# Optimization experiments

Measured on AMD Instinct MI355X. Metric: run time of the kernel, lower is better.

Reference implementation:

```python
import jax, jax.numpy as jnp
import numpy as np

COMMITMENT_COST = 0.25
NUM_EMBEDDINGS = 4096
EMBEDDING_DIM = 256


def setup_inputs() -> dict:
    key = jax.random.key(0)
    kx, ke = jax.random.split(key)
    x = jax.random.normal(kx, (64, 1024, EMBEDDING_DIM), dtype=jnp.float32)
    # nn.Embedding weight initialized uniform(-1/K, 1/K)
    emb = jax.random.uniform(ke, (NUM_EMBEDDINGS, EMBEDDING_DIM), dtype=jnp.float32,
                             minval=-1.0 / NUM_EMBEDDINGS, maxval=1.0 / NUM_EMBEDDINGS)
    return {"x": x, "emb": emb}


def reference(x, emb):
    D = emb.shape[1]
    flat_x = x.reshape(-1, D)                                    # [N, D]
    distances = (jnp.sum(flat_x * flat_x, axis=1, keepdims=True)
                 - 2.0 * flat_x @ emb.T
                 + jnp.sum(emb * emb, axis=1))
    indices = jnp.argmin(distances, axis=1)                      # [N]
    quantized = emb[indices].reshape(x.shape)                    # [..., D]
    e_latent_loss = jnp.mean((jax.lax.stop_gradient(quantized) - x) ** 2)
    q_latent_loss = jnp.mean((quantized - jax.lax.stop_gradient(x)) ** 2)
    loss = q_latent_loss + COMMITMENT_COST * e_latent_loss
    # straight-through estimator
    quantized = x + jax.lax.stop_gradient(quantized - x)
    return quantized, loss, indices[:, None]
```

## Files before the change

### kernel.cpp

```cpp
#include <hip/hip_runtime.h>
#include <math.h>

#define DIMD 256
#define KCODES 4096
#define NROWS 65536
#define QN (NROWS * DIMD)

constexpr int P1_BM = 64;
constexpr int P1_BN = 128;
constexpr int NT    = KCODES / P1_BN;
constexpr float TAU2 = 7.5e-4f;
constexpr float TAU2B = TAU2 + 1e-5f;
constexpr int CAP   = 48;
constexpr int NS    = 8;

typedef __attribute__((ext_vector_type(8))) short bf16x8;
typedef __attribute__((ext_vector_type(4))) float f32x4;

__device__ __forceinline__ unsigned short f2bf(float f) {
    unsigned int u = __builtin_bit_cast(unsigned int, f);
    u += 0x7fffu + ((u >> 16) & 1u);
    return (unsigned short)(u >> 16);
}

__device__ __forceinline__ float opaque(float v) {
    asm volatile("" : "+v"(v));
    return v;
}

__device__ __forceinline__ void gload_lds16(const void* g, void* l) {
    __builtin_amdgcn_global_load_lds(
        (const __attribute__((address_space(1))) unsigned int*)g,
        (__attribute__((address_space(3))) unsigned int*)l, 16, 0, 0);
}

__device__ __forceinline__ float np_sumsq_256(const float* __restrict__ p) {
    float total = 0.0f;
    #pragma unroll
    for (int half = 0; half < 2; ++half) {
        const float* b = p + half * 128;
        float r[8];
        #pragma unroll
        for (int j = 0; j < 8; ++j) {
            const float v = b[j];
            r[j] = opaque(v * v);
        }
        for (int i = 8; i < 128; i += 8) {
            #pragma unroll
            for (int j = 0; j < 8; ++j) {
                const float v = b[i + j];
                r[j] += opaque(v * v);
            }
        }
        const float res = ((r[0] + r[1]) + (r[2] + r[3])) + ((r[4] + r[5]) + (r[6] + r[7]));
        total = (half == 0) ? res : (total + res);
    }
    return total;
}

__global__ void sx_kernel(const float* __restrict__ x, float* __restrict__ sx) {
    const int row = blockIdx.x * blockDim.x + threadIdx.x;
    sx[row] = np_sumsq_256(x + (size_t)row * DIMD);
}

__global__ void se_kernel(const float* __restrict__ emb, float* __restrict__ se) {
    const int k = blockIdx.x * blockDim.x + threadIdx.x;
    se[k] = np_sumsq_256(emb + (size_t)k * DIMD);
}

__global__ void conv_emb_kernel(const float* __restrict__ emb, unsigned short* __restrict__ embh) {
    const int i = blockIdx.x * blockDim.x + threadIdx.x;
    const float4 v = ((const float4*)emb)[i];
    ushort4 h;
    h.x = f2bf(v.x); h.y = f2bf(v.y); h.z = f2bf(v.z); h.w = f2bf(v.w);
    ((ushort4*)embh)[i] = h;
}

__global__ __launch_bounds__(256, 2)
void pass1_kernel(const float* __restrict__ x, const unsigned short* __restrict__ embh,
                  unsigned int* __restrict__ cand, int* __restrict__ cnt_out) {
    __shared__ unsigned short Bs[2][8192];
    __shared__ float part[4][32];
    __shared__ float tilemax[P1_BM];
    __shared__ int   cnts[P1_BM];

    const int t    = threadIdx.x;
    const int w    = t >> 6;
    const int lane = t & 63;
    const int quad = lane >> 4;
    const int lm   = lane & 15;
    const int wr   = w >> 1;
    const int wc   = w & 1;
    const int row0 = blockIdx.x * P1_BM;

    if (t < P1_BM) cnts[t] = 0;

    bf16x8 afr[2][8];
    #pragma unroll
    for (int f = 0; f < 2; ++f) {
        const float* xr = x + (size_t)(row0 + wr * 32 + f * 16 + lm) * DIMD + quad * 8;
        #pragma unroll
        for (int c = 0; c < 8; ++c) {
            const float4 v0 = *(const float4*)(xr + c * 32);
            const float4 v1 = *(const float4*)(xr + c * 32 + 4);
            bf16x8 h;
            h[0] = (short)f2bf(v0.x); h[1] = (short)f2bf(v0.y);
            h[2] = (short)f2bf(v0.z); h[3] = (short)f2bf(v0.w);
            h[4] = (short)f2bf(v1.x); h[5] = (short)f2bf(v1.y);
            h[6] = (short)f2bf(v1.z); h[7] = (short)f2bf(v1.w);
            afr[f][c] = h;
        }
    }

    auto stage = [&](int buf, int m) {
        const int c0  = (m >> 2) * P1_BN;
        const int kcb = (m & 3) * 64;
        #pragma unroll
        for (int i = 0; i < 4; ++i) {
            const int seg  = i * 4 + w;
            const int code = seg * 8 + (lane >> 3);
            const int kk   = ((lane & 7) ^ ((lane >> 3) & 7)) * 8;
            const unsigned short* src = embh + (size_t)(c0 + code) * DIMD + kcb + kk;
            gload_lds16(src, &Bs[buf][seg * 512]);
        }
    };

    stage(0, 0);
    asm volatile("s_waitcnt vmcnt(0)" ::: "memory");
    __syncthreads();

    float rmg[2][4];
    #pragma unroll
    for (int f = 0; f < 2; ++f)
        #pragma unroll
        for (int reg = 0; reg < 4; ++reg) rmg[f][reg] = -INFINITY;

    int buf = 0;
    for (int tile = 0; tile < NT; ++tile) {
        const int c0 = tile * P1_BN;
        f32x4 acc[2][4];
        #pragma unroll
        for (int f = 0; f < 2; ++f)
            #pragma unroll
            for (int g = 0; g < 4; ++g) acc[f][g] = (f32x4){0.f, 0.f, 0.f, 0.f};

        #pragma unroll
        for (int kb = 0; kb < 4; ++kb) {
            const int m = tile * 4 + kb;
            if (m < NT * 4 - 1) stage(buf ^ 1, m + 1);

            #pragma unroll
            for (int ks = 0; ks < 2; ++ks) {
                bf16x8 b[4];
                #pragma unroll
                for (int g = 0; g < 4; ++g) {
                    const int j = wc * 64 + g * 16 + lm;
                    b[g] = *(const bf16x8*)
                        &Bs[buf][j * 64 + ((((ks << 2) + quad) ^ (lm & 7)) << 3)];
                }
                #pragma unroll
                for (int f = 0; f < 2; ++f)
                    #pragma unroll
                    for (int g = 0; g < 4; ++g)
                        acc[f][g] = __builtin_amdgcn_mfma_f32_16x16x32_bf16(
                            afr[f][kb * 2 + ks], b[g], acc[f][g], 0, 0, 0);
            }

            if (kb == 3) {
                #pragma unroll
                for (int f = 0; f < 2; ++f) {
                    f32x4 mm4;
                    #pragma unroll
                    for (int reg = 0; reg < 4; ++reg) {
                        float mm = fmaxf(fmaxf(acc[f][0][reg], acc[f][1][reg]),
                                         fmaxf(acc[f][2][reg], acc[f][3][reg]));
                        #pragma unroll
                        for (int off = 1; off < 16; off <<= 1)
                            mm = fmaxf(mm, __shfl_xor(mm, off, 64));
                        mm4[reg] = mm;
                    }
                    if (lm == 0)
                        *(f32x4*)&part[w][f * 16 + quad * 4] = mm4;
                }
            }

            asm volatile("s_waitcnt vmcnt(0)" ::: "memory");
            __syncthreads();
            buf ^= 1;
        }

        if (t < P1_BM) {
            const int trh = t >> 5, loc = t & 31;
            tilemax[t] = fmaxf(part[trh * 2][loc], part[trh * 2 + 1][loc]);
        }
        __syncthreads();

        #pragma unroll
        for (int f = 0; f < 2; ++f) {
            const f32x4 tm = *(const f32x4*)&tilemax[wr * 32 + f * 16 + quad * 4];
            #pragma unroll
            for (int reg = 0; reg < 4; ++reg) {
                rmg[f][reg] = fmaxf(rmg[f][reg], tm[reg]);
                const float thr = rmg[f][reg] - TAU2;
                const int r = wr * 32 + f * 16 + quad * 4 + reg;
                #pragma unroll
                for (int g = 0; g < 4; ++g) {
                    const float dv = acc[f][g][reg];
                    if (dv > thr) {
                        const int slot = atomicAdd(&cnts[r], 1);
                        if (slot < CAP) {
                            const unsigned int ub =
                                __builtin_bit_cast(unsigned int, fmaxf(dv, 0.0f));
                            cand[(size_t)(row0 + r) * CAP + slot] =
                                (ub & 0xFFFFF000u) |
                                (unsigned int)(c0 + wc * 64 + g * 16 + lm);
                        }
                    }
                }
            }
        }
    }
    __syncthreads();
    if (t < P1_BM) cnt_out[row0 + t] = (cnts[t] > CAP) ? -1 : cnts[t];
}

__global__ __launch_bounds__(256, 2)
void pass2_kernel(const float* __restrict__ x, const float* __restrict__ emb,
                  const float* __restrict__ sx, const float* __restrict__ se,
                  const unsigned int* __restrict__ cand, const int* __restrict__ cnt,
                  float* __restrict__ out, float* __restrict__ partial) {
    __shared__ float4 xsh[4][64];
    __shared__ float4 esh[4][NS][65];
    const int w = threadIdx.x >> 6, lane = threadIdx.x & 63;
    const int row = blockIdx.x * 4 + w;
    const int n = cnt[row];
    const float sxr = sx[row];
    const float4* emb4 = (const float4*)emb;

    const float4 myx = ((const float4*)(x + (size_t)row * DIMD))[lane];
    xsh[w][lane] = myx;
    const float4* xs4 = &xsh[w][0];

    float bestd = INFINITY;
    int   bestc = 0x7fffffff;

    if (n >= 1 && n <= CAP) {
        float dtil = -INFINITY;
        int   code = 0;
        if (lane < n) {
            const unsigned int word = cand[(size_t)row * CAP + lane];
            dtil = __builtin_bit_cast(float, word & 0xFFFFF000u);
            code = (int)(word & 0xFFFu);
        }
        float mx = dtil;
        #pragma unroll
        for (int off = 1; off < 64; off <<= 1)
            mx = fmaxf(mx, __shfl_xor(mx, off, 64));
        const bool active = (lane < n) && (dtil > mx - TAU2B);
        const unsigned long long mask = __ballot(active);
        const int nact = __popcll(mask);
        const int slot = __popcll(mask & ((1ull << lane) - 1ull));
        unsigned long long mm = mask;
        const int ns = nact < NS ? nact : NS;
        for (int i = 0; i < ns; ++i) {
            const int li = __ffsll((unsigned long long)mm) - 1;
            mm &= mm - 1;
            const int bc = __shfl(code, li, 64);
            esh[w][i][lane] = emb4[(size_t)bc * 64 + lane];
        }
        if (active) {
            float a = 0.0f;
            if (slot < NS) {
                const float4* ep4 = &esh[w][slot][0];
                #pragma unroll
                for (int d4 = 0; d4 < DIMD / 4; ++d4) {
                    const float4 ev = ep4[d4];
                    const float4 xv = xs4[d4];
                    a = fmaf(xv.x, ev.x, a);
                    a = fmaf(xv.y, ev.y, a);
                    a = fmaf(xv.z, ev.z, a);
                    a = fmaf(xv.w, ev.w, a);
                }
            } else {
                const float4* ep4 = (const float4*)(emb + (size_t)code * DIMD);
                #pragma unroll
                for (int d4 = 0; d4 < DIMD / 4; ++d4) {
                    const float4 ev = ep4[d4];
                    const float4 xv = xs4[d4];
                    a = fmaf(xv.x, ev.x, a);
                    a = fmaf(xv.y, ev.y, a);
                    a = fmaf(xv.z, ev.z, a);
                    a = fmaf(xv.w, ev.w, a);
                }
            }
            const float t1 = sxr - 2.0f * a;
            bestd = t1 + se[code];
            bestc = code;
        }
    } else {
        for (int c = lane; c < KCODES; c += 64) {
            const float* ep = emb + (size_t)c * DIMD;
            float a = 0.0f;
            for (int d4 = 0; d4 < DIMD / 4; ++d4) {
                const float4 xv = xs4[d4];
                const float4 ev = ((const float4*)ep)[d4];
                a = fmaf(xv.x, ev.x, a);
                a = fmaf(xv.y, ev.y, a);
                a = fmaf(xv.z, ev.z, a);
                a = fmaf(xv.w, ev.w, a);
            }
            const float t1 = sxr - 2.0f * a;
            const float dd = t1 + se[c];
            if (dd < bestd || (dd == bestd && c < bestc)) { bestd = dd; bestc = c; }
        }
    }
    #pragma unroll
    for (int off = 32; off > 0; off >>= 1) {
        const float od = __shfl_down(bestd, off, 64);
        const int   oc = __shfl_down(bestc, off, 64);
        if (od < bestd || (od == bestd && oc < bestc)) { bestd = od; bestc = oc; }
    }
    bestc = __shfl(bestc, 0, 64);

    const float4 e4 = emb4[(size_t)bestc * 64 + lane];
    ((float4*)(out + (size_t)row * DIMD))[lane] = e4;
    const float dx = e4.x - myx.x, dy = e4.y - myx.y,
                dz = e4.z - myx.z, dw = e4.w - myx.w;
    float s = dx * dx + dy * dy + dz * dz + dw * dw;
    #pragma unroll
    for (int off = 32; off > 0; off >>= 1) s += __shfl_down(s, off, 64);
    if (lane == 0) {
        partial[row] = s;
        out[QN + 1 + row] = (float)bestc;
    }
}

__global__ void loss_reduce_kernel(const float* __restrict__ partial, float* __restrict__ out) {
    const int t = threadIdx.x;
    double s = 0.0;
    for (int i = t; i < NROWS; i += 256) s += (double)partial[i];
    __shared__ double tsum[256];
    tsum[t] = s;
    __syncthreads();
    #pragma unroll
    for (int off = 128; off > 0; off >>= 1) {
        if (t < off) tsum[t] += tsum[t + off];
        __syncthreads();
    }
    if (t == 0) out[QN] = (float)(tsum[0] * (1.25 / (double)QN));
}

extern "C" void kernel_launch(void* const* d_in, const int* in_sizes, int n_in,
                              void* d_out, int out_size, void* d_ws, size_t ws_size,
                              hipStream_t stream) {
    const float* x   = (const float*)d_in[0];
    const float* emb = (const float*)d_in[1];
    float* out = (float*)d_out;

    char* ws = (char*)d_ws;
    unsigned short* embh = (unsigned short*)ws;           ws += (size_t)KCODES * DIMD * 2;
    float* sx  = (float*)ws;                              ws += (size_t)NROWS * 4;
    float* se  = (float*)ws;                              ws += (size_t)KCODES * 4;
    unsigned int* cand = (unsigned int*)ws;               ws += (size_t)NROWS * CAP * 4;
    int*   cnt  = (int*)ws;                               ws += (size_t)NROWS * 4;
    float* partial = (float*)ws;

    conv_emb_kernel<<<KCODES * DIMD / 4 / 256, 256, 0, stream>>>(emb, embh);
    sx_kernel<<<NROWS / 256, 256, 0, stream>>>(x, sx);
    se_kernel<<<KCODES / 256, 256, 0, stream>>>(emb, se);
    pass1_kernel<<<NROWS / P1_BM, 256, 0, stream>>>(x, embh, cand, cnt);
    pass2_kernel<<<NROWS / 4, 256, 0, stream>>>(x, emb, sx, se, cand, cnt, out, partial);
    loss_reduce_kernel<<<1, 256, 0, stream>>>(partial, out);
}
```

Measured before the change: 793.3 us.

## Triple-buffer pass1 LDS staging, cooperative row norms, LDS-staged pass2 candidates

Pass1 moves from a double to a triple LDS buffer that prefetches two k-blocks ahead, using partial vmcnt waits so global loads overlap the MFMA work. The sx/se norm kernels now use 8 lanes per row with shuffle reductions in place of one thread per row, which gives coalesced loads. Pass2 loads candidate embeddings into LDS with global_load_lds, drops the padding column, reuses the staged winning row for the output, and raises occupancy to 4 blocks. The norm reduction order changes, which may shift sums slightly versus the numpy-matching order, and the partial vmcnt counts have to match the number of loads issued per stage.

```diff
diff --git a/kernel.cpp b/kernel.cpp
--- a/kernel.cpp
+++ b/kernel.cpp
@@ -17,6 +17,10 @@
 typedef __attribute__((ext_vector_type(8))) short bf16x8;
 typedef __attribute__((ext_vector_type(4))) float f32x4;
 
+#define VM8() asm volatile("s_waitcnt vmcnt(8)" ::: "memory")
+#define VM4() asm volatile("s_waitcnt vmcnt(4)" ::: "memory")
+#define VM0() asm volatile("s_waitcnt vmcnt(0)" ::: "memory")
+
 __device__ __forceinline__ unsigned short f2bf(float f) {
     unsigned int u = __builtin_bit_cast(unsigned int, f);
     u += 0x7fffu + ((u >> 16) & 1u);
@@ -34,38 +38,50 @@
         (__attribute__((address_space(3))) unsigned int*)l, 16, 0, 0);
 }
 
-__device__ __forceinline__ float np_sumsq_256(const float* __restrict__ p) {
+__global__ void sx_kernel(const float* __restrict__ x, float* __restrict__ sx) {
+    const int j   = threadIdx.x & 7;
+    const int row = blockIdx.x * 32 + (threadIdx.x >> 3);
+    const float* p = x + (size_t)row * DIMD;
     float total = 0.0f;
     #pragma unroll
     for (int half = 0; half < 2; ++half) {
         const float* b = p + half * 128;
-        float r[8];
-        #pragma unroll
-        for (int j = 0; j < 8; ++j) {
-            const float v = b[j];
-            r[j] = opaque(v * v);
-        }
+        const float v0 = b[j];
+        float r = opaque(v0 * v0);
+        #pragma unroll
         for (int i = 8; i < 128; i += 8) {
-            #pragma unroll
-            for (int j = 0; j < 8; ++j) {
-                const float v = b[i + j];
-                r[j] += opaque(v * v);
-            }
-        }
-        const float res = ((r[0] + r[1]) + (r[2] + r[3])) + ((r[4] + r[5]) + (r[6] + r[7]));
+            const float v = b[i + j];
+            r += opaque(v * v);
+        }
+        const float s1  = r  + __shfl_xor(r, 1, 64);
+        const float s2  = s1 + __shfl_xor(s1, 2, 64);
+        const float res = s2 + __shfl_xor(s2, 4, 64);
         total = (half == 0) ? res : (total + res);
     }
-    return total;
-}
-
-__global__ void sx_kernel(const float* __restrict__ x, float* __restrict__ sx) {
-    const int row = blockIdx.x * blockDim.x + threadIdx.x;
-    sx[row] = np_sumsq_256(x + (size_t)row * DIMD);
+    if (j == 0) sx[row] = total;
 }
 
 __global__ void se_kernel(const float* __restrict__ emb, float* __restrict__ se) {
-    const int k = blockIdx.x * blockDim.x + threadIdx.x;
-    se[k] = np_sumsq_256(emb + (size_t)k * DIMD);
+    const int j   = threadIdx.x & 7;
+    const int row = blockIdx.x * 32 + (threadIdx.x >> 3);
+    const float* p = emb + (size_t)row * DIMD;
+    float total = 0.0f;
+    #pragma unroll
+    for (int half = 0; half < 2; ++half) {
+        const float* b = p + half * 128;
+        const float v0 = b[j];
+        float r = opaque(v0 * v0);
+        #pragma unroll
+        for (int i = 8; i < 128; i += 8) {
+            const float v = b[i + j];
+            r += opaque(v * v);
+        }
+        const float s1  = r  + __shfl_xor(r, 1, 64);
+        const float s2  = s1 + __shfl_xor(s1, 2, 64);
+        const float res = s2 + __shfl_xor(s2, 4, 64);
+        total = (half == 0) ? res : (total + res);
+    }
+    if (j == 0) se[row] = total;
 }
 
 __global__ void conv_emb_kernel(const float* __restrict__ emb, unsigned short* __restrict__ embh) {
@@ -79,7 +95,7 @@
 __global__ __launch_bounds__(256, 2)
 void pass1_kernel(const float* __restrict__ x, const unsigned short* __restrict__ embh,
                   unsigned int* __restrict__ cand, int* __restrict__ cnt_out) {
-    __shared__ unsigned short Bs[2][8192];
+    __shared__ unsigned short Bs[3][8192];
     __shared__ float part[4][32];
     __shared__ float tilemax[P1_BM];
     __shared__ int   cnts[P1_BM];
@@ -126,8 +142,8 @@
     };
 
     stage(0, 0);
-    asm volatile("s_waitcnt vmcnt(0)" ::: "memory");
-    __syncthreads();
+    stage(1, 1);
+    int bc = 0;
 
     float rmg[2][4];
     #pragma unroll
@@ -135,7 +151,6 @@
         #pragma unroll
         for (int reg = 0; reg < 4; ++reg) rmg[f][reg] = -INFINITY;
 
-    int buf = 0;
     for (int tile = 0; tile < NT; ++tile) {
         const int c0 = tile * P1_BN;
         f32x4 acc[2][4];
@@ -147,7 +162,18 @@
         #pragma unroll
         for (int kb = 0; kb < 4; ++kb) {
             const int m = tile * 4 + kb;
-            if (m < NT * 4 - 1) stage(buf ^ 1, m + 1);
+            __syncthreads();
+            int st = bc + 2; if (st >= 3) st -= 3;
+            if (tile < NT - 1) {
+                stage(st, m + 2);
+                VM8();
+            } else {
+                if (kb == 0) { stage(st, m + 2); VM8(); }
+                else if (kb == 1) { stage(st, m + 2); VM8(); }
+                else if (kb == 2) { VM4(); }
+                else { VM0(); }
+            }
+            __syncthreads();
 
             #pragma unroll
             for (int ks = 0; ks < 2; ++ks) {
@@ -156,7 +182,7 @@
                 for (int g = 0; g < 4; ++g) {
                     const int j = wc * 64 + g * 16 + lm;
                     b[g] = *(const bf16x8*)
-                        &Bs[buf][j * 64 + ((((ks << 2) + quad) ^ (lm & 7)) << 3)];
+                        &Bs[bc][j * 64 + ((((ks << 2) + quad) ^ (lm & 7)) << 3)];
                 }
                 #pragma unroll
                 for (int f = 0; f < 2; ++f)
@@ -183,12 +209,10 @@
                         *(f32x4*)&part[w][f * 16 + quad * 4] = mm4;
                 }
             }
-
-            asm volatile("s_waitcnt vmcnt(0)" ::: "memory");
-            __syncthreads();
-            buf ^= 1;
-        }
-
+            bc = (bc == 2) ? 0 : bc + 1;
+        }
+
+        __syncthreads();
         if (t < P1_BM) {
             const int trh = t >> 5, loc = t & 31;
             tilemax[t] = fmaxf(part[trh * 2][loc], part[trh * 2 + 1][loc]);
@@ -219,18 +243,19 @@
                 }
             }
         }
+        VM0();
     }
     __syncthreads();
     if (t < P1_BM) cnt_out[row0 + t] = (cnts[t] > CAP) ? -1 : cnts[t];
 }
 
-__global__ __launch_bounds__(256, 2)
+__global__ __launch_bounds__(256, 4)
 void pass2_kernel(const float* __restrict__ x, const float* __restrict__ emb,
                   const float* __restrict__ sx, const float* __restrict__ se,
                   const unsigned int* __restrict__ cand, const int* __restrict__ cnt,
                   float* __restrict__ out, float* __restrict__ partial) {
     __shared__ float4 xsh[4][64];
-    __shared__ float4 esh[4][NS][65];
+    __shared__ float4 esh[4][NS][64];
     const int w = threadIdx.x >> 6, lane = threadIdx.x & 63;
     const int row = blockIdx.x * 4 + w;
     const int n = cnt[row];
@@ -243,6 +268,7 @@
 
     float bestd = INFINITY;
     int   bestc = 0x7fffffff;
+    int   wslot = 0x7fffffff;
 
     if (n >= 1 && n <= CAP) {
         float dtil = -INFINITY;
@@ -263,11 +289,12 @@
         unsigned long long mm = mask;
         const int ns = nact < NS ? nact : NS;
         for (int i = 0; i < ns; ++i) {
-            const int li = __ffsll((unsigned long long)mm) - 1;
+            const int li = __ffsll(mm) - 1;
             mm &= mm - 1;
             const int bc = __shfl(code, li, 64);
-            esh[w][i][lane] = emb4[(size_t)bc * 64 + lane];
-        }
+            gload_lds16(emb4 + (size_t)bc * 64 + lane, &esh[w][i][0]);
+        }
+        VM0();
         if (active) {
             float a = 0.0f;
             if (slot < NS) {
@@ -282,7 +309,7 @@
                     a = fmaf(xv.w, ev.w, a);
                 }
             } else {
-                const float4* ep4 = (const float4*)(emb + (size_t)code * DIMD);
+                const float4* ep4 = emb4 + (size_t)code * 64;
                 #pragma unroll
                 for (int d4 = 0; d4 < DIMD / 4; ++d4) {
                     const float4 ev = ep4[d4];
@@ -296,6 +323,7 @@
             const float t1 = sxr - 2.0f * a;
             bestd = t1 + se[code];
             bestc = code;
+            wslot = slot;
         }
     } else {
         for (int c = lane; c < KCODES; c += 64) {
@@ -318,11 +346,16 @@
     for (int off = 32; off > 0; off >>= 1) {
         const float od = __shfl_down(bestd, off, 64);
         const int   oc = __shfl_down(bestc, off, 64);
-        if (od < bestd || (od == bestd && oc < bestc)) { bestd = od; bestc = oc; }
+        const int   os = __shfl_down(wslot, off, 64);
+        if (od < bestd || (od == bestd && oc < bestc)) {
+            bestd = od; bestc = oc; wslot = os;
+        }
     }
     bestc = __shfl(bestc, 0, 64);
-
-    const float4 e4 = emb4[(size_t)bestc * 64 + lane];
+    wslot = __shfl(wslot, 0, 64);
+
+    const float4 e4 = (wslot < NS) ? esh[w][wslot][lane]
+                                   : emb4[(size_t)bestc * 64 + lane];
     ((float4*)(out + (size_t)row * DIMD))[lane] = e4;
     const float dx = e4.x - myx.x, dy = e4.y - myx.y,
                 dz = e4.z - myx.z, dw = e4.w - myx.w;
@@ -366,8 +399,8 @@
     float* partial = (float*)ws;
 
     conv_emb_kernel<<<KCODES * DIMD / 4 / 256, 256, 0, stream>>>(emb, embh);
-    sx_kernel<<<NROWS / 256, 256, 0, stream>>>(x, sx);
-    se_kernel<<<KCODES / 256, 256, 0, stream>>>(emb, se);
+    sx_kernel<<<NROWS / 32, 256, 0, stream>>>(x, sx);
+    se_kernel<<<KCODES / 32, 256, 0, stream>>>(emb, se);
     pass1_kernel<<<NROWS / P1_BM, 256, 0, stream>>>(x, embh, cand, cnt);
     pass2_kernel<<<NROWS / 4, 256, 0, stream>>>(x, emb, sx, se, cand, cnt, out, partial);
     loss_reduce_kernel<<<1, 256, 0, stream>>>(partial, out);
```

After: 782.4 us. No clear change (-1.4%).
